# Kernel tuning notes

Hardware: AMD Instinct MI355X
Metric: run time of the kernel (lower is better)

The kernel has to match this reference:

```python
import jax, jax.numpy as jnp
import numpy as np
import math

D_MODEL = 512
N_HEADS = 8
D_HEAD = D_MODEL // N_HEADS
B, T = 2, 2048


def quant_linear(x, W, b, bitwidth):
    # BitNet-b1.58 style: ternary weights (per-tensor absmean scale),
    # activations quantized to signed `bitwidth` with per-token absmax scale.
    ws = jnp.mean(jnp.abs(W)) + 1e-5
    Wq = jnp.clip(jnp.round(W / ws), -1.0, 1.0)
    Qb = 2.0 ** (bitwidth - 1) - 1.0
    xs = Qb / (jnp.max(jnp.abs(x), axis=-1, keepdims=True) + 1e-5)
    xq = jnp.clip(jnp.round(x * xs), -Qb, Qb)
    return (xq @ W.T if False else jnp.einsum('...i,oi->...o', xq, Wq)) * (ws / xs) + b


def layer_norm(x, g, b, eps=1e-5):
    mu = jnp.mean(x, axis=-1, keepdims=True)
    var = jnp.mean(jnp.square(x - mu), axis=-1, keepdims=True)
    return (x - mu) * jax.lax.rsqrt(var + eps) * g + b


def rel_shift(x):
    # x: [B, H, T, T]
    b, h, t1, t2 = x.shape
    x = jnp.pad(x, ((0, 0), (0, 0), (0, 0), (1, 0)))  # [B,H,T,T+1]
    x = x.reshape(b, h, t2 + 1, t1)[:, :, 1:, :]
    return x.reshape(b, h, t1, t2)


def setup_inputs() -> dict:
    key = jax.random.key(0)
    ks = jax.random.split(key, 16)
    s = 0.02
    inp = {
        'x': jax.random.normal(ks[0], (B, T, D_MODEL), jnp.float32),
        'mask': jnp.ones((B, T, T), jnp.int32),
        'pos_emb': jax.random.normal(ks[1], (1, T, D_MODEL), jnp.float32),
        'ln_g': jnp.ones((D_MODEL,), jnp.float32),
        'ln_b': jnp.zeros((D_MODEL,), jnp.float32),
        'Wq': jax.random.normal(ks[2], (D_MODEL, D_MODEL), jnp.float32) * s,
        'bq': jnp.zeros((D_MODEL,), jnp.float32),
        'Wk': jax.random.normal(ks[3], (D_MODEL, D_MODEL), jnp.float32) * s,
        'bk': jnp.zeros((D_MODEL,), jnp.float32),
        'Wv': jax.random.normal(ks[4], (D_MODEL, D_MODEL), jnp.float32) * s,
        'bv': jnp.zeros((D_MODEL,), jnp.float32),
        'Wp': jax.random.normal(ks[5], (D_MODEL, D_MODEL), jnp.float32) * s,
        'bp': jnp.zeros((D_MODEL,), jnp.float32),
        'Wo': jax.random.normal(ks[6], (D_MODEL, D_MODEL), jnp.float32) * s,
        'bo': jnp.zeros((D_MODEL,), jnp.float32),
        'pos_bias_u': jax.random.normal(ks[7], (N_HEADS, D_HEAD), jnp.float32) * 0.01,
        'pos_bias_v': jax.random.normal(ks[8], (N_HEADS, D_HEAD), jnp.float32) * 0.01,
        'bitwidth': 8,
    }
    return inp


def reference(x, mask, pos_emb, ln_g, ln_b, Wq, bq, Wk, bk, Wv, bv, Wp, bp, Wo, bo, pos_bias_u, pos_bias_v, bitwidth):
    b, t, c = x.shape
    y = layer_norm(x, ln_g, ln_b)
    # projections -> [B, H, T, Dh]
    Q = quant_linear(y, Wq, bq, bitwidth).reshape(b, t, N_HEADS, D_HEAD).transpose(0, 2, 1, 3)
    K = quant_linear(y, Wk, bk, bitwidth).reshape(b, t, N_HEADS, D_HEAD).transpose(0, 2, 1, 3)
    V = quant_linear(y, Wv, bv, bitwidth).reshape(b, t, N_HEADS, D_HEAD).transpose(0, 2, 1, 3)
    p = quant_linear(pos_emb, Wp, bp, bitwidth).reshape(1, t, N_HEADS, D_HEAD).transpose(0, 2, 1, 3)
    Qu = Q + pos_bias_u[None, :, None, :]
    Qv = Q + pos_bias_v[None, :, None, :]
    matrix_ac = jnp.einsum('bhqd,bhkd->bhqk', Qu, K)
    matrix_bd = rel_shift(jnp.einsum('bhqd,xhkd->bhqk', Qv, p))
    scores = (matrix_ac + matrix_bd) / math.sqrt(D_HEAD)
    scores = jnp.where(mask[:, None, :, :] == 0, -jnp.inf, scores)
    A = jnp.nan_to_num(jax.nn.softmax(scores, axis=-1), nan=0.0)
    H = jnp.einsum('bhqk,bhkd->bhqd', A, V).transpose(0, 2, 1, 3).reshape(b, t, c)
    H = quant_linear(H, Wo, bo, bitwidth)
    H = H * mask[:, :, 0:1].astype(H.dtype)  # seq mask
    return x + H
```

## Files before the change

kernel.cpp:

```cpp
#include <hip/hip_runtime.h>
#include <math.h>

#define TT 2048
#define DMODEL 512
#define NHEADS 8
#define DHEAD 64
#define NBATCH 2
#define MTOK (NBATCH*TT)
#define NSPLIT 4
#define SC 0.18033688011112042f

typedef unsigned short u16;
typedef unsigned int u32;
typedef __bf16 bf16x8 __attribute__((ext_vector_type(8)));
typedef float f32x4 __attribute__((ext_vector_type(4)));
typedef short s16x4 __attribute__((ext_vector_type(4)));
typedef short s16x8 __attribute__((ext_vector_type(8)));
typedef unsigned short u16x4 __attribute__((ext_vector_type(4)));
typedef int s32x4 __attribute__((ext_vector_type(4)));

#define MFMA16(a,b,c) __builtin_amdgcn_mfma_f32_16x16x32_bf16(a,b,c,0,0,0)
#define MFMA_PV(a,b,c) __builtin_amdgcn_mfma_f32_16x16x16bf16_1k(a,b,c,0,0,0)

__device__ __forceinline__ u16 f2b(float f){
  u32 x = __float_as_uint(f);
  x = x + 0x7fffu + ((x >> 16) & 1u);
  return (u16)(x >> 16);
}
__device__ __forceinline__ float b2f(u16 u){
  return __uint_as_float(((u32)u) << 16);
}
__device__ __forceinline__ u32 cvtpk(float lo, float hi){
  u32 d; asm("v_cvt_pk_bf16_f32 %0, %1, %2" : "=v"(d) : "v"(lo), "v"(hi)); return d;
}
__device__ __forceinline__ size_t fidx(int t, int d){
  return ((size_t)((t>>4)*16 + (d>>5)))*512
       + (size_t)(((((d>>3)&3)*16) + (t&15))*8 + (d&7));
}

__global__ __launch_bounds__(256) void wprep1_kernel(
    const float* __restrict__ W0, const float* __restrict__ W1,
    const float* __restrict__ W2, const float* __restrict__ W3,
    const float* __restrict__ W4, float* __restrict__ partial)
{
  int widx = blockIdx.y;
  const float* W = (widx==0)?W0:(widx==1)?W1:(widx==2)?W2:(widx==3)?W3:W4;
  size_t base = (size_t)blockIdx.x * 4096;
  int tid = threadIdx.x;
  float s = 0.f;
  for (int i = tid; i < 4096; i += 256) s += fabsf(W[base + i]);
  __shared__ float red[256];
  red[tid] = s; __syncthreads();
  for (int o = 128; o > 0; o >>= 1){ if (tid < o) red[tid] += red[tid+o]; __syncthreads(); }
  if (tid == 0) partial[widx*64 + blockIdx.x] = red[0];
}

__global__ __launch_bounds__(256) void wprep2_kernel(
    const float* __restrict__ W0, const float* __restrict__ W1,
    const float* __restrict__ W2, const float* __restrict__ W3,
    const float* __restrict__ W4, const float* __restrict__ partial,
    float* __restrict__ wsv, u16* __restrict__ wt)
{
  int widx = blockIdx.y;
  const float* W = (widx==0)?W0:(widx==1)?W1:(widx==2)?W2:(widx==3)?W3:W4;
  __shared__ float red[64];
  int tid = threadIdx.x;
  if (tid < 64) red[tid] = partial[widx*64 + tid];
  __syncthreads();
  for (int o = 32; o > 0; o >>= 1){ if (tid < o) red[tid] += red[tid+o]; __syncthreads(); }
  float ws = red[0] * (1.0f/262144.0f) + 1e-5f;
  if (blockIdx.x == 0 && tid == 0) wsv[widx] = ws;
  int base = blockIdx.x * 1024;
  for (int i = tid; i < 1024; i += 256){
    int idx = base + i;
    int n = idx >> 9, k = idx & 511;
    float v = rintf(W[idx] / ws);
    v = fminf(fmaxf(v, -1.f), 1.f);
    wt[(size_t)widx*262144 + fidx(n, k)] = f2b(v);
  }
}

__global__ __launch_bounds__(256) void lnq_kernel(
    const float* __restrict__ x, const float* __restrict__ g, const float* __restrict__ b,
    const int* __restrict__ bwp, u16* __restrict__ xq, float* __restrict__ stok)
{
  int t = blockIdx.x;
  const float* xr = x + (size_t)t * DMODEL;
  int tid = threadIdx.x;
  float v0 = xr[tid], v1 = xr[tid + 256];
  __shared__ float red[256];
  red[tid] = v0 + v1; __syncthreads();
  for (int o=128;o>0;o>>=1){ if(tid<o) red[tid]+=red[tid+o]; __syncthreads(); }
  float mu = red[0] * (1.0f/512.0f);
  __syncthreads();
  float d0 = v0 - mu, d1 = v1 - mu;
  red[tid] = d0*d0 + d1*d1; __syncthreads();
  for (int o=128;o>0;o>>=1){ if(tid<o) red[tid]+=red[tid+o]; __syncthreads(); }
  float var = red[0] * (1.0f/512.0f);
  __syncthreads();
  float rs = rsqrtf(var + 1e-5f);
  float y0 = d0*rs*g[tid] + b[tid];
  float y1 = d1*rs*g[tid+256] + b[tid+256];
  red[tid] = fmaxf(fabsf(y0), fabsf(y1)); __syncthreads();
  for (int o=128;o>0;o>>=1){ if(tid<o) red[tid]=fmaxf(red[tid],red[tid+o]); __syncthreads(); }
  float amax = red[0];
  float Qb = (float)((1 << (bwp[0]-1)) - 1);
  float xs = Qb / (amax + 1e-5f);
  if (tid == 0) stok[t] = (amax + 1e-5f) / Qb;
  float q0 = fminf(fmaxf(rintf(y0 * xs), -Qb), Qb);
  float q1 = fminf(fmaxf(rintf(y1 * xs), -Qb), Qb);
  xq[fidx(t, tid)]       = f2b(q0);
  xq[fidx(t, tid + 256)] = f2b(q1);
}

__global__ __launch_bounds__(256) void quant_kernel(
    const float* __restrict__ src, const int* __restrict__ bwp,
    u16* __restrict__ xq, float* __restrict__ stok)
{
  int t = blockIdx.x;
  const float* xr = src + (size_t)t * DMODEL;
  int tid = threadIdx.x;
  float v0 = xr[tid], v1 = xr[tid + 256];
  __shared__ float red[256];
  red[tid] = fmaxf(fabsf(v0), fabsf(v1)); __syncthreads();
  for (int o=128;o>0;o>>=1){ if(tid<o) red[tid]=fmaxf(red[tid],red[tid+o]); __syncthreads(); }
  float amax = red[0];
  float Qb = (float)((1 << (bwp[0]-1)) - 1);
  float xs = Qb / (amax + 1e-5f);
  if (tid == 0) stok[t] = (amax + 1e-5f) / Qb;
  float q0 = fminf(fmaxf(rintf(v0 * xs), -Qb), Qb);
  float q1 = fminf(fmaxf(rintf(v1 * xs), -Qb), Qb);
  xq[fidx(t, tid)]       = f2b(q0);
  xq[fidx(t, tid + 256)] = f2b(q1);
}

__global__ __launch_bounds__(256) void maskflag_kernel(const int* __restrict__ mask, int* __restrict__ rowflag){
  int row = blockIdx.x;
  int tid = threadIdx.x;
  int ok = 1;
  const int* mr = mask + (size_t)row * TT;
  for (int i = tid; i < TT; i += 256) ok &= (mr[i] != 0);
  __shared__ int red[256];
  red[tid] = ok; __syncthreads();
  for (int o=128;o>0;o>>=1){ if(tid<o) red[tid] &= red[tid+o]; __syncthreads(); }
  if (tid == 0) rowflag[row] = red[0];
}

__global__ __launch_bounds__(256) void qkvgemm_kernel(
    const u16* __restrict__ Af, const u16* __restrict__ wtf,
    const float* __restrict__ stok, const float* __restrict__ wsv,
    const float* __restrict__ bq, const float* __restrict__ bk, const float* __restrict__ bv,
    const float* __restrict__ pbu, const float* __restrict__ pbv,
    u16* __restrict__ Qu, u16* __restrict__ Qv, u16* __restrict__ Kf, u16* __restrict__ Vf)
{
  int w = threadIdx.x >> 6, lane = threadIdx.x & 63;
  int g = lane >> 4, li = lane & 15;
  int mb = blockIdx.y*64 + w*16;
  int nb = blockIdx.x*64;
  int widx = nb >> 9;
  int ntb = (nb & 511) >> 4;
  f32x4 acc[4] = {{0,0,0,0},{0,0,0,0},{0,0,0,0},{0,0,0,0}};
  const u16* Ab = Af + (size_t)(mb >> 4)*16*512 + lane*8;
  const u16* Bb = wtf + (size_t)widx*262144 + (size_t)ntb*16*512 + lane*8;
  for (int kb = 0; kb < 16; kb++){
    bf16x8 a = *(const bf16x8*)(Ab + kb*512);
#pragma unroll
    for (int f = 0; f < 4; f++){
      bf16x8 bb = *(const bf16x8*)(Bb + (f*16 + kb)*512);
      acc[f] = MFMA16(a, bb, acc[f]);
    }
  }
  float ws = wsv[widx];
  const float* bias = (widx==0)?bq:(widx==1)?bk:bv;
  float sc[4];
#pragma unroll
  for (int r=0;r<4;r++) sc[r] = ws * stok[mb + 4*g + r];
#pragma unroll
  for (int f=0;f<4;f++){
    int n = nb + 16*f + li;
    int nq = n & 511;
    float bn = bias[nq];
#pragma unroll
    for (int r=0;r<4;r++){
      int m = mb + 4*g + r;
      float val = acc[f][r]*sc[r] + bn;
      int bb_ = m >> 11, t = m & (TT-1); int h = nq >> 6, d = nq & 63;
      int bh = bb_*NHEADS + h;
      if (widx == 0){
        size_t o = (((size_t)bh)*TT + t)*DHEAD + d;
        Qu[o] = f2b((val + pbu[nq])*SC);
        Qv[o] = f2b(val + pbv[nq]);
      } else if (widx == 1){
        size_t o = (((size_t)bh*128 + (t>>4))*2 + (d>>5))*512
                 + (size_t)((((d>>3)&3)*16 + (t&15))*8 + (d&7));
        Kf[o] = f2b(val);
      } else {
        size_t o = (((size_t)bh*128 + (t>>4))*2 + (d>>5))*512
                 + (size_t)(((((t>>2)&3)*16) + (d&15))*8 + (((d>>4)&1)*4) + (t&3));
        Vf[o] = f2b(val);
      }
    }
  }
}

template<int NF>
__global__ __launch_bounds__(256) void qgemm_kernel(
    const u16* __restrict__ Af, const u16* __restrict__ Wtf,
    const float* __restrict__ stok, const float* __restrict__ wsv, int widx,
    const float* __restrict__ bias, int mode,
    u16* __restrict__ outA, float* __restrict__ outF,
    const float* __restrict__ xin, const int* __restrict__ mask)
{
  int w = threadIdx.x >> 6, lane = threadIdx.x & 63;
  int g = lane >> 4, li = lane & 15;
  int mb = blockIdx.y*64 + w*16;
  int nb = blockIdx.x*(16*NF);
  f32x4 acc[NF];
#pragma unroll
  for (int f=0; f<NF; f++) acc[f] = (f32x4){0,0,0,0};
  const u16* Ab = Af + (size_t)(mb >> 4)*16*512 + lane*8;
  const u16* Bb = Wtf + (size_t)(nb >> 4)*16*512 + lane*8;
  for (int kb = 0; kb < 16; kb++){
    bf16x8 a = *(const bf16x8*)(Ab + kb*512);
#pragma unroll
    for (int f = 0; f < NF; f++){
      bf16x8 bb = *(const bf16x8*)(Bb + (f*16 + kb)*512);
      acc[f] = MFMA16(a, bb, acc[f]);
    }
  }
  float ws = wsv[widx];
  float sc[4];
#pragma unroll
  for (int r=0;r<4;r++) sc[r] = ws * stok[mb + 4*g + r];
#pragma unroll
  for (int f=0;f<NF;f++){
    int n = nb + 16*f + li;
    float bn = bias[n];
#pragma unroll
    for (int r=0;r<4;r++){
      int m = mb + 4*g + r;
      float val = acc[f][r]*sc[r] + bn;
      if (mode == 3){
        int h = n >> 6, d = n & 63;
        size_t o = (((size_t)h*128 + (m>>4))*2 + (d>>5))*512
                 + (size_t)((((d>>3)&3)*16 + (m&15))*8 + (d&7));
        outA[o] = f2b(val);
      } else {
        int bb_ = m >> 11, t = m & (TT-1);
        float mv = (float)mask[((size_t)bb_*TT + t)*TT];
        outF[(size_t)m*DMODEL + n] = xin[(size_t)m*DMODEL + n] + val*mv;
      }
    }
  }
}

__global__ __launch_bounds__(256) void flash_kernel(
    const u16* __restrict__ Qu, const u16* __restrict__ Qv,
    const u16* __restrict__ Kf, const u16* __restrict__ Vf,
    const u16* __restrict__ Pf,
    const int* __restrict__ mask, const int* __restrict__ rowflag,
    u16* __restrict__ Opart, float* __restrict__ Mpart, float* __restrict__ Lpart)
{
  __shared__ float bdt[64][68];
  int w = threadIdx.x >> 6, lane = threadIdx.x & 63;
  int g = lane >> 4, li = lane & 15;
  int bh = blockIdx.y; int b = bh >> 3, h = bh & 7;
  int z = blockIdx.z;
  int qb = blockIdx.x*64;
  int qt = qb + 16*w;
  int q  = qt + li;

  const u16* qrow = Qu + ((size_t)bh*TT + q)*DHEAD;
  bf16x8 qu0 = *(const bf16x8*)(qrow + 8*g);
  bf16x8 qu1 = *(const bf16x8*)(qrow + 32 + 8*g);
  const u16* vr0 = Qv + ((size_t)bh*TT + q)*DHEAD;
  bf16x8 qv00 = *(const bf16x8*)(vr0 + 8*g);
  bf16x8 qv01 = *(const bf16x8*)(vr0 + 32 + 8*g);
  int q1 = (q < TT-1) ? (q+1) : (TT-1);
  const u16* vr1 = Qv + ((size_t)bh*TT + q1)*DHEAD;
  bf16x8 qv10 = *(const bf16x8*)(vr1 + 8*g);
  bf16x8 qv11 = *(const bf16x8*)(vr1 + 32 + 8*g);

  float* bdrow = &bdt[16*w + li][0];

  f32x4 acc[4] = {{0,0,0,0},{0,0,0,0},{0,0,0,0},{0,0,0,0}};
  float mrun = -3e38f, lrun = 0.f;
  int rf = rowflag[b*TT + q];
  bool needmask = (__all(rf) == 0);

  const u16* kfb = Kf + (size_t)bh*128*1024;
  const u16* vfb = Vf + (size_t)bh*128*1024;
  const u16* Pl  = Pf + (size_t)h*128*1024 + lane*8;
  const int* maskq = mask + ((size_t)b*TT + q)*TT;

  int kofs_lo = 4*g - (2047 - qt - li);
  int kofs_up = 4*g + qt + li + 2;

  int kbeg = z * (TT/NSPLIT);
  for (int k0 = kbeg; k0 < kbeg + TT/NSPLIT; k0 += 64){
    int kb = k0 >> 4;
    f32x4 s[4];
#pragma unroll
    for (int kc = 0; kc < 4; kc++){
      const u16* kp = kfb + (size_t)(kb + kc)*1024 + lane*8;
      f32x4 t_ = {0,0,0,0};
      t_ = MFMA16(*(const bf16x8*)(kp),       qu0, t_);
      t_ = MFMA16(*(const bf16x8*)(kp + 512), qu1, t_);
      s[kc] = t_;
    }
    {
      int JL0 = (k0 + 2032 - qt) & ~15;
      int jl1 = (k0 + 2110 - qt) & ~15;
      int JL1 = (jl1 < 2032) ? jl1 : 2032;
      for (int jt = JL0; jt <= JL1; jt += 16){
        const u16* pp = Pl + jt*64;
        f32x4 c = {0,0,0,0};
        c = MFMA16(*(const bf16x8*)(pp),       qv00, c);
        c = MFMA16(*(const bf16x8*)(pp + 512), qv01, c);
        int kp2 = jt + kofs_lo - k0;
#pragma unroll
        for (int r = 0; r < 4; r++){
          int kpr = kp2 + r;
          if ((unsigned)kpr < 64u) bdrow[kpr] = c[r]*SC;
        }
      }
      int ju0 = (k0 - qt - 17) & ~15;
      int JU0 = (ju0 > 0) ? ju0 : 0;
      int ju1 = (k0 + 61 - qt) & ~15;
      int JU1 = (ju1 < 2032) ? ju1 : 2032;
      for (int jt = JU0; jt <= JU1; jt += 16){
        const u16* pp = Pl + jt*64;
        f32x4 c = {0,0,0,0};
        c = MFMA16(*(const bf16x8*)(pp),       qv10, c);
        c = MFMA16(*(const bf16x8*)(pp + 512), qv11, c);
        int kp2 = jt + kofs_up - k0;
#pragma unroll
        for (int r = 0; r < 4; r++){
          int kpr = kp2 + r;
          if ((unsigned)kpr < 64u) bdrow[kpr] = c[r]*SC;
        }
      }
      int kd = q + 1 - k0;
      if ((unsigned)kd < 64u) bdrow[kd] = 0.f;
    }
#pragma unroll
    for (int kc = 0; kc < 4; kc++){
      f32x4 bd4 = *(const f32x4*)(&bdrow[16*kc + 4*g]);
#pragma unroll
      for (int r = 0; r < 4; r++) s[kc][r] += bd4[r];
    }
    if (needmask && !rf){
#pragma unroll
      for (int kc = 0; kc < 4; kc++){
        s32x4 mv = *(const s32x4*)(maskq + k0 + 16*kc + 4*g);
#pragma unroll
        for (int r = 0; r < 4; r++)
          if (mv[r] == 0) s[kc][r] = -3e38f;
      }
    }
    float tm = s[0][0];
#pragma unroll
    for (int kc = 0; kc < 4; kc++)
#pragma unroll
      for (int r = 0; r < 4; r++) tm = fmaxf(tm, s[kc][r]);
    tm = fmaxf(tm, __shfl_xor(tm, 16));
    tm = fmaxf(tm, __shfl_xor(tm, 32));
    float mn;
    if (__all(tm <= mrun)){
      mn = mrun;
    } else {
      mn = fmaxf(mrun, tm);
      float fscq = __builtin_amdgcn_exp2f(mrun - mn);
      mrun = mn;
      lrun *= fscq;
#pragma unroll
      for (int r = 0; r < 4; r++){
        float fr = __shfl(fscq, 4*g + r);
        acc[0][r] *= fr; acc[1][r] *= fr; acc[2][r] *= fr; acc[3][r] *= fr;
      }
    }
    float ps = 0.f;
    s16x4 pk[4];
#pragma unroll
    for (int kc = 0; kc < 4; kc++){
      float p0 = __builtin_amdgcn_exp2f(s[kc][0] - mn);
      float p1 = __builtin_amdgcn_exp2f(s[kc][1] - mn);
      float p2 = __builtin_amdgcn_exp2f(s[kc][2] - mn);
      float p3 = __builtin_amdgcn_exp2f(s[kc][3] - mn);
      ps += (p0 + p1) + (p2 + p3);
      union { u32 w[2]; s16x4 v; } u_;
      u_.w[0] = cvtpk(p0, p1);
      u_.w[1] = cvtpk(p2, p3);
      pk[kc] = u_.v;
    }
    ps += __shfl_xor(ps, 16);
    ps += __shfl_xor(ps, 32);
    lrun += ps;
#pragma unroll
    for (int kc = 0; kc < 4; kc++){
      const u16* vp = vfb + (size_t)(kb + kc)*1024 + lane*8;
      bf16x8 v0 = *(const bf16x8*)(vp);
      bf16x8 v1 = *(const bf16x8*)(vp + 512);
      s16x8 w0 = (s16x8)v0, w1 = (s16x8)v1;
      acc[0] = MFMA_PV(pk[kc], __builtin_shufflevector(w0, w0, 0,1,2,3), acc[0]);
      acc[1] = MFMA_PV(pk[kc], __builtin_shufflevector(w0, w0, 4,5,6,7), acc[1]);
      acc[2] = MFMA_PV(pk[kc], __builtin_shufflevector(w1, w1, 0,1,2,3), acc[2]);
      acc[3] = MFMA_PV(pk[kc], __builtin_shufflevector(w1, w1, 4,5,6,7), acc[3]);
    }
  }
#pragma unroll
  for (int r = 0; r < 4; r++){
    size_t o = ((size_t)(b*TT + qb + 16*w + 4*g + r)*NSPLIT + z)*DMODEL + h*DHEAD + li;
    Opart[o]      = f2b(acc[0][r]);
    Opart[o + 16] = f2b(acc[1][r]);
    Opart[o + 32] = f2b(acc[2][r]);
    Opart[o + 48] = f2b(acc[3][r]);
  }
  if (lane < 16){
    size_t mo = ((size_t)(b*TT + qt + li)*NSPLIT + z)*NHEADS + h;
    Mpart[mo] = mrun;
    Lpart[mo] = lrun;
  }
}

__global__ __launch_bounds__(256) void merge_kernel(
    const u16* __restrict__ Opart, const float* __restrict__ Mpart, const float* __restrict__ Lpart,
    const int* __restrict__ bwp, u16* __restrict__ xq, float* __restrict__ stok)
{
  int tok = blockIdx.x, tid = threadIdx.x;
  __shared__ float scl[NSPLIT][NHEADS];
  if (tid < NHEADS){
    int h = tid;
    float ms[NSPLIT], ls[NSPLIT];
#pragma unroll
    for (int s = 0; s < NSPLIT; s++){
      ms[s] = Mpart[((size_t)tok*NSPLIT + s)*NHEADS + h];
      ls[s] = Lpart[((size_t)tok*NSPLIT + s)*NHEADS + h];
    }
    float mst = ms[0];
#pragma unroll
    for (int s = 1; s < NSPLIT; s++) mst = fmaxf(mst, ms[s]);
    float sc_[NSPLIT]; float lst = 0.f;
#pragma unroll
    for (int s = 0; s < NSPLIT; s++){
      sc_[s] = __builtin_amdgcn_exp2f(ms[s] - mst);
      lst += ls[s]*sc_[s];
    }
    float inv = (lst > 0.f) ? 1.0f/lst : 0.f;
#pragma unroll
    for (int s = 0; s < NSPLIT; s++) scl[s][h] = sc_[s]*inv;
  }
  __syncthreads();
  float hv[2];
#pragma unroll
  for (int j = 0; j < 2; j++){
    int idx = tid + 256*j;
    int h = idx >> 6;
    float a = 0.f;
#pragma unroll
    for (int s = 0; s < NSPLIT; s++)
      a += b2f(Opart[((size_t)tok*NSPLIT + s)*DMODEL + idx]) * scl[s][h];
    hv[j] = a;
  }
  __shared__ float red[256];
  red[tid] = fmaxf(fabsf(hv[0]), fabsf(hv[1])); __syncthreads();
  for (int o=128;o>0;o>>=1){ if(tid<o) red[tid]=fmaxf(red[tid],red[tid+o]); __syncthreads(); }
  float amax = red[0];
  float Qb = (float)((1 << (bwp[0]-1)) - 1);
  float xs = Qb / (amax + 1e-5f);
  if (tid == 0) stok[tok] = (amax + 1e-5f) / Qb;
#pragma unroll
  for (int j = 0; j < 2; j++){
    int idx = tid + 256*j;
    float qv = fminf(fmaxf(rintf(hv[j] * xs), -Qb), Qb);
    xq[fidx(tok, idx)] = f2b(qv);
  }
}

extern "C" void kernel_launch(void* const* d_in, const int* in_sizes, int n_in,
                              void* d_out, int out_size, void* d_ws, size_t ws_size,
                              hipStream_t stream) {
  const float* x    = (const float*)d_in[0];
  const int*   mask = (const int*)  d_in[1];
  const float* pos  = (const float*)d_in[2];
  const float* lng  = (const float*)d_in[3];
  const float* lnb  = (const float*)d_in[4];
  const float* Wq   = (const float*)d_in[5];
  const float* bq   = (const float*)d_in[6];
  const float* Wk   = (const float*)d_in[7];
  const float* bk   = (const float*)d_in[8];
  const float* Wv   = (const float*)d_in[9];
  const float* bv   = (const float*)d_in[10];
  const float* Wp   = (const float*)d_in[11];
  const float* bp   = (const float*)d_in[12];
  const float* Wo   = (const float*)d_in[13];
  const float* bo   = (const float*)d_in[14];
  const float* pbu  = (const float*)d_in[15];
  const float* pbv  = (const float*)d_in[16];
  const int*   bwp  = (const int*)  d_in[17];
  float* out = (float*)d_out;

  char* wsb = (char*)d_ws;
  size_t off = 0;
  auto alloc = [&](size_t nbytes)->char* {
    char* p = wsb + off;
    off = (off + nbytes + 255) & ~(size_t)255;
    return p;
  };
  float* partial = (float*)alloc(5*64*sizeof(float));
  float* wsv     = (float*)alloc(5*sizeof(float));
  u16*   wt      = (u16*)  alloc((size_t)5*262144*2);
  float* stok_y  = (float*)alloc(MTOK*sizeof(float));
  float* stok_p  = (float*)alloc(TT*sizeof(float));
  u16*   Qu      = (u16*)  alloc((size_t)16*TT*DHEAD*2);
  u16*   Qv      = (u16*)  alloc((size_t)16*TT*DHEAD*2);
  u16*   Kf      = (u16*)  alloc((size_t)16*TT*DHEAD*2);
  u16*   Vf      = (u16*)  alloc((size_t)16*TT*DHEAD*2);
  u16*   Pf      = (u16*)  alloc((size_t)NHEADS*TT*DHEAD*2);
  u16*   pool    = (u16*)  alloc((size_t)MTOK*NSPLIT*DMODEL*2);
  u16*   xq_y    = pool;
  u16*   xq_p    = pool + (size_t)MTOK*DMODEL;
  u16*   Opart   = pool;
  float* Mpart   = (float*)alloc((size_t)MTOK*NSPLIT*NHEADS*sizeof(float));
  float* Lpart   = (float*)alloc((size_t)MTOK*NSPLIT*NHEADS*sizeof(float));
  u16*   xq_H    = (u16*)  alloc((size_t)MTOK*DMODEL*2);
  float* stok_H  = (float*)alloc(MTOK*sizeof(float));
  int*   rowflag = (int*)  alloc(MTOK*sizeof(int));
  if (off > ws_size) return;

  wprep1_kernel<<<dim3(64,5), 256, 0, stream>>>(Wq, Wk, Wv, Wp, Wo, partial);
  wprep2_kernel<<<dim3(256,5), 256, 0, stream>>>(Wq, Wk, Wv, Wp, Wo, partial, wsv, wt);
  lnq_kernel<<<MTOK, 256, 0, stream>>>(x, lng, lnb, bwp, xq_y, stok_y);
  quant_kernel<<<TT, 256, 0, stream>>>(pos, bwp, xq_p, stok_p);
  maskflag_kernel<<<MTOK, 256, 0, stream>>>(mask, rowflag);
  qkvgemm_kernel<<<dim3(24,64), 256, 0, stream>>>(xq_y, wt, stok_y, wsv, bq, bk, bv, pbu, pbv,
                                                  Qu, Qv, Kf, Vf);
  qgemm_kernel<2><<<dim3(16,32), 256, 0, stream>>>(xq_p, wt + (size_t)3*262144, stok_p, wsv, 3, bp, 3,
                                                   Pf, nullptr, nullptr, nullptr);
  flash_kernel<<<dim3(32,16,NSPLIT), 256, 0, stream>>>(Qu, Qv, Kf, Vf, Pf, mask, rowflag,
                                                       Opart, Mpart, Lpart);
  merge_kernel<<<MTOK, 256, 0, stream>>>(Opart, Mpart, Lpart, bwp, xq_H, stok_H);
  qgemm_kernel<2><<<dim3(16,64), 256, 0, stream>>>(xq_H, wt + (size_t)4*262144, stok_H, wsv, 4, bo, 4,
                                                   nullptr, out, x, mask);
}
```

Baseline: 213.3 us.

## Compute rel-shift positional band over 128-key strips with swizzled LDS buffer

```diff
diff --git a/kernel.cpp b/kernel.cpp
--- a/kernel.cpp
+++ b/kernel.cpp
@@ -16,7 +16,6 @@
 typedef float f32x4 __attribute__((ext_vector_type(4)));
 typedef short s16x4 __attribute__((ext_vector_type(4)));
 typedef short s16x8 __attribute__((ext_vector_type(8)));
-typedef unsigned short u16x4 __attribute__((ext_vector_type(4)));
 typedef int s32x4 __attribute__((ext_vector_type(4)));
 
 #define MFMA16(a,b,c) __builtin_amdgcn_mfma_f32_16x16x32_bf16(a,b,c,0,0,0)
@@ -261,7 +260,7 @@
     const int* __restrict__ mask, const int* __restrict__ rowflag,
     u16* __restrict__ Opart, float* __restrict__ Mpart, float* __restrict__ Lpart)
 {
-  __shared__ float bdt[64][68];
+  __shared__ float bdl[64*128];
   int w = threadIdx.x >> 6, lane = threadIdx.x & 63;
   int g = lane >> 4, li = lane & 15;
   int bh = blockIdx.y; int b = bh >> 3, h = bh & 7;
@@ -269,6 +268,8 @@
   int qb = blockIdx.x*64;
   int qt = qb + 16*w;
   int q  = qt + li;
+  int rowbase = (16*w + li)*128;
+  int swz = (li & 7) << 2;
 
   const u16* qrow = Qu + ((size_t)bh*TT + q)*DHEAD;
   bf16x8 qu0 = *(const bf16x8*)(qrow + 8*g);
@@ -281,8 +282,6 @@
   bf16x8 qv10 = *(const bf16x8*)(vr1 + 8*g);
   bf16x8 qv11 = *(const bf16x8*)(vr1 + 32 + 8*g);
 
-  float* bdrow = &bdt[16*w + li][0];
-
   f32x4 acc[4] = {{0,0,0,0},{0,0,0,0},{0,0,0,0},{0,0,0,0}};
   float mrun = -3e38f, lrun = 0.f;
   int rf = rowflag[b*TT + q];
@@ -297,120 +296,124 @@
   int kofs_up = 4*g + qt + li + 2;
 
   int kbeg = z * (TT/NSPLIT);
-  for (int k0 = kbeg; k0 < kbeg + TT/NSPLIT; k0 += 64){
-    int kb = k0 >> 4;
-    f32x4 s[4];
-#pragma unroll
-    for (int kc = 0; kc < 4; kc++){
-      const u16* kp = kfb + (size_t)(kb + kc)*1024 + lane*8;
-      f32x4 t_ = {0,0,0,0};
-      t_ = MFMA16(*(const bf16x8*)(kp),       qu0, t_);
-      t_ = MFMA16(*(const bf16x8*)(kp + 512), qu1, t_);
-      s[kc] = t_;
-    }
+  for (int ks = kbeg; ks < kbeg + TT/NSPLIT; ks += 128){
     {
-      int JL0 = (k0 + 2032 - qt) & ~15;
-      int jl1 = (k0 + 2110 - qt) & ~15;
+      int JL0 = (ks + 2032 - qt) & ~15;
+      int jl1 = (ks + 2174 - qt) & ~15;
       int JL1 = (jl1 < 2032) ? jl1 : 2032;
       for (int jt = JL0; jt <= JL1; jt += 16){
         const u16* pp = Pl + jt*64;
         f32x4 c = {0,0,0,0};
         c = MFMA16(*(const bf16x8*)(pp),       qv00, c);
         c = MFMA16(*(const bf16x8*)(pp + 512), qv01, c);
-        int kp2 = jt + kofs_lo - k0;
+        int sbase = jt + kofs_lo - ks;
 #pragma unroll
         for (int r = 0; r < 4; r++){
-          int kpr = kp2 + r;
-          if ((unsigned)kpr < 64u) bdrow[kpr] = c[r]*SC;
+          int s_ = sbase + r;
+          if ((unsigned)s_ < 128u) bdl[rowbase + (s_ ^ swz)] = c[r]*SC;
         }
       }
-      int ju0 = (k0 - qt - 17) & ~15;
+      int ju0 = (ks - qt - 17) & ~15;
       int JU0 = (ju0 > 0) ? ju0 : 0;
-      int ju1 = (k0 + 61 - qt) & ~15;
+      int ju1 = (ks + 125 - qt) & ~15;
       int JU1 = (ju1 < 2032) ? ju1 : 2032;
       for (int jt = JU0; jt <= JU1; jt += 16){
         const u16* pp = Pl + jt*64;
         f32x4 c = {0,0,0,0};
         c = MFMA16(*(const bf16x8*)(pp),       qv10, c);
         c = MFMA16(*(const bf16x8*)(pp + 512), qv11, c);
-        int kp2 = jt + kofs_up - k0;
+        int sbase = jt + kofs_up - ks;
 #pragma unroll
         for (int r = 0; r < 4; r++){
-          int kpr = kp2 + r;
-          if ((unsigned)kpr < 64u) bdrow[kpr] = c[r]*SC;
+          int s_ = sbase + r;
+          if ((unsigned)s_ < 128u) bdl[rowbase + (s_ ^ swz)] = c[r]*SC;
         }
       }
-      int kd = q + 1 - k0;
-      if ((unsigned)kd < 64u) bdrow[kd] = 0.f;
-    }
-#pragma unroll
-    for (int kc = 0; kc < 4; kc++){
-      f32x4 bd4 = *(const f32x4*)(&bdrow[16*kc + 4*g]);
-#pragma unroll
-      for (int r = 0; r < 4; r++) s[kc][r] += bd4[r];
-    }
-    if (needmask && !rf){
+      int kd = q + 1 - ks;
+      if ((unsigned)kd < 128u) bdl[rowbase + (kd ^ swz)] = 0.f;
+    }
+#pragma unroll
+    for (int sub = 0; sub < 2; sub++){
+      int k0 = ks + 64*sub;
+      int kb = k0 >> 4;
+      f32x4 s[4];
 #pragma unroll
       for (int kc = 0; kc < 4; kc++){
-        s32x4 mv = *(const s32x4*)(maskq + k0 + 16*kc + 4*g);
-#pragma unroll
-        for (int r = 0; r < 4; r++)
-          if (mv[r] == 0) s[kc][r] = -3e38f;
-      }
-    }
-    float tm = s[0][0];
-#pragma unroll
-    for (int kc = 0; kc < 4; kc++)
-#pragma unroll
-      for (int r = 0; r < 4; r++) tm = fmaxf(tm, s[kc][r]);
-    tm = fmaxf(tm, __shfl_xor(tm, 16));
-    tm = fmaxf(tm, __shfl_xor(tm, 32));
-    float mn;
-    if (__all(tm <= mrun)){
-      mn = mrun;
-    } else {
-      mn = fmaxf(mrun, tm);
-      float fscq = __builtin_amdgcn_exp2f(mrun - mn);
-      mrun = mn;
-      lrun *= fscq;
-#pragma unroll
-      for (int r = 0; r < 4; r++){
-        float fr = __shfl(fscq, 4*g + r);
-        acc[0][r] *= fr; acc[1][r] *= fr; acc[2][r] *= fr; acc[3][r] *= fr;
-      }
-    }
-    float ps = 0.f;
-    s16x4 pk[4];
-#pragma unroll
-    for (int kc = 0; kc < 4; kc++){
-      float p0 = __builtin_amdgcn_exp2f(s[kc][0] - mn);
-      float p1 = __builtin_amdgcn_exp2f(s[kc][1] - mn);
-      float p2 = __builtin_amdgcn_exp2f(s[kc][2] - mn);
-      float p3 = __builtin_amdgcn_exp2f(s[kc][3] - mn);
-      ps += (p0 + p1) + (p2 + p3);
-      union { u32 w[2]; s16x4 v; } u_;
-      u_.w[0] = cvtpk(p0, p1);
-      u_.w[1] = cvtpk(p2, p3);
-      pk[kc] = u_.v;
-    }
-    ps += __shfl_xor(ps, 16);
-    ps += __shfl_xor(ps, 32);
-    lrun += ps;
-#pragma unroll
-    for (int kc = 0; kc < 4; kc++){
-      const u16* vp = vfb + (size_t)(kb + kc)*1024 + lane*8;
-      bf16x8 v0 = *(const bf16x8*)(vp);
-      bf16x8 v1 = *(const bf16x8*)(vp + 512);
-      s16x8 w0 = (s16x8)v0, w1 = (s16x8)v1;
-      acc[0] = MFMA_PV(pk[kc], __builtin_shufflevector(w0, w0, 0,1,2,3), acc[0]);
-      acc[1] = MFMA_PV(pk[kc], __builtin_shufflevector(w0, w0, 4,5,6,7), acc[1]);
-      acc[2] = MFMA_PV(pk[kc], __builtin_shufflevector(w1, w1, 0,1,2,3), acc[2]);
-      acc[3] = MFMA_PV(pk[kc], __builtin_shufflevector(w1, w1, 4,5,6,7), acc[3]);
+        const u16* kp = kfb + (size_t)(kb + kc)*1024 + lane*8;
+        f32x4 t_ = {0,0,0,0};
+        t_ = MFMA16(*(const bf16x8*)(kp),       qu0, t_);
+        t_ = MFMA16(*(const bf16x8*)(kp + 512), qu1, t_);
+        s[kc] = t_;
+      }
+#pragma unroll
+      for (int kc = 0; kc < 4; kc++){
+        f32x4 bd4 = *(const f32x4*)(&bdl[rowbase + ((64*sub + 16*kc + 4*g) ^ swz)]);
+#pragma unroll
+        for (int r = 0; r < 4; r++) s[kc][r] += bd4[r];
+      }
+      if (needmask && !rf){
+#pragma unroll
+        for (int kc = 0; kc < 4; kc++){
+          s32x4 mv = *(const s32x4*)(maskq + k0 + 16*kc + 4*g);
+#pragma unroll
+          for (int r = 0; r < 4; r++)
+            if (mv[r] == 0) s[kc][r] = -3e38f;
+        }
+      }
+      float tm = s[0][0];
+#pragma unroll
+      for (int kc = 0; kc < 4; kc++)
+#pragma unroll
+        for (int r = 0; r < 4; r++) tm = fmaxf(tm, s[kc][r]);
+      tm = fmaxf(tm, __shfl_xor(tm, 16));
+      tm = fmaxf(tm, __shfl_xor(tm, 32));
+      float mn;
+      if (__all(tm <= mrun)){
+        mn = mrun;
+      } else {
+        mn = fmaxf(mrun, tm);
+        float fscq = __builtin_amdgcn_exp2f(mrun - mn);
+        mrun = mn;
+        lrun *= fscq;
+#pragma unroll
+        for (int r = 0; r < 4; r++){
+          float fr = __shfl(fscq, 4*g + r);
+          acc[0][r] *= fr; acc[1][r] *= fr; acc[2][r] *= fr; acc[3][r] *= fr;
+        }
+      }
+      float ps = 0.f;
+      s16x4 pk[4];
+#pragma unroll
+      for (int kc = 0; kc < 4; kc++){
+        float p0 = __builtin_amdgcn_exp2f(s[kc][0] - mn);
+        float p1 = __builtin_amdgcn_exp2f(s[kc][1] - mn);
+        float p2 = __builtin_amdgcn_exp2f(s[kc][2] - mn);
+        float p3 = __builtin_amdgcn_exp2f(s[kc][3] - mn);
+        ps += (p0 + p1) + (p2 + p3);
+        union { u32 w[2]; s16x4 v; } u_;
+        u_.w[0] = cvtpk(p0, p1);
+        u_.w[1] = cvtpk(p2, p3);
+        pk[kc] = u_.v;
+      }
+      ps += __shfl_xor(ps, 16);
+      ps += __shfl_xor(ps, 32);
+      lrun += ps;
+#pragma unroll
+      for (int kc = 0; kc < 4; kc++){
+        const u16* vp = vfb + (size_t)(kb + kc)*1024 + lane*8;
+        bf16x8 v0 = *(const bf16x8*)(vp);
+        bf16x8 v1 = *(const bf16x8*)(vp + 512);
+        s16x8 w0 = (s16x8)v0, w1 = (s16x8)v1;
+        acc[0] = MFMA_PV(pk[kc], __builtin_shufflevector(w0, w0, 0,1,2,3), acc[0]);
+        acc[1] = MFMA_PV(pk[kc], __builtin_shufflevector(w0, w0, 4,5,6,7), acc[1]);
+        acc[2] = MFMA_PV(pk[kc], __builtin_shufflevector(w1, w1, 0,1,2,3), acc[2]);
+        acc[3] = MFMA_PV(pk[kc], __builtin_shufflevector(w1, w1, 4,5,6,7), acc[3]);
+      }
     }
   }
 #pragma unroll
   for (int r = 0; r < 4; r++){
-    size_t o = ((size_t)(b*TT + qb + 16*w + 4*g + r)*NSPLIT + z)*DMODEL + h*DHEAD + li;
+    size_t o = ((size_t)(b*TT + qt + 4*g + r)*NSPLIT + z)*DMODEL + h*DHEAD + li;
     Opart[o]      = f2b(acc[0][r]);
     Opart[o + 16] = f2b(acc[1][r]);
     Opart[o + 32] = f2b(acc[2][r]);
```

Result: faster. 203.7 us (-4.5%).
